# Kernel optimization log

Hardware: AMD Instinct MI355X
Metric: run time of the kernel (lower is better)

The kernel has to match this reference:

```python
import jax, jax.numpy as jnp
import numpy as np

N = 100000   # nodes
E = 300000   # edges
D_IN = 128   # input feature dim
H = 256      # hidden dim
L = 4        # GIN layers
G = 512      # graphs in batch
BN_EPS = 1e-5


def setup_inputs() -> dict:
    key = jax.random.key(0)
    ks = jax.random.split(key, 12)
    s = 0.02
    return {
        "x": jax.random.normal(ks[0], (N, D_IN), jnp.float32),
        "edge_index": jax.random.randint(ks[1], (2, E), 0, N, dtype=jnp.int32),
        "batch": jnp.sort(jax.random.randint(ks[2], (N,), 0, G, dtype=jnp.int32)),
        "W_in": jax.random.normal(ks[3], (D_IN, H), jnp.float32) * s,
        "b_in": jnp.zeros((H,), jnp.float32),
        "eps": jnp.zeros((L,), jnp.float32),           # GINConv train_eps init = 0
        "W1": jax.random.normal(ks[4], (L, H, 2 * H), jnp.float32) * s,
        "b1": jnp.zeros((L, 2 * H), jnp.float32),
        "W2": jax.random.normal(ks[5], (L, 2 * H, H), jnp.float32) * s,
        "b2": jnp.zeros((L, H), jnp.float32),
        "gamma": jnp.ones((L, H), jnp.float32),
        "beta": jnp.zeros((L, H), jnp.float32),
        "Wp1": jax.random.normal(ks[6], (H, H // 2), jnp.float32) * s,
        "bp1": jnp.zeros((H // 2,), jnp.float32),
        "Wp2": jax.random.normal(ks[7], (H // 2, 1), jnp.float32) * s,
        "bp2": jnp.zeros((1,), jnp.float32),
    }


def reference(x, edge_index, batch, W_in, b_in, eps, W1, b1, W2, b2,
              gamma, beta, Wp1, bp1, Wp2, bp2):
    src, dst = edge_index[0], edge_index[1]

    # input projection + relu
    h = jax.nn.relu(x @ W_in + b_in)  # [N, H]

    def layer(h, p):
        e, w1, bb1, w2, bb2, g, bt = p
        # GINConv: sum-aggregate neighbor messages at destination nodes
        agg = jax.ops.segment_sum(h[src], dst, num_segments=N)  # [N, H]
        z = (1.0 + e) * h + agg
        # GIN MLP: H -> 2H -> H
        z = jax.nn.relu(z @ w1 + bb1) @ w2 + bb2
        # BatchNorm over node dim (training-mode batch statistics, biased var)
        mu = jnp.mean(z, axis=0)
        var = jnp.var(z, axis=0)
        z = g * (z - mu) * jax.lax.rsqrt(var + BN_EPS) + bt
        return jax.nn.relu(z), None

    h, _ = jax.lax.scan(layer, h, (eps, W1, b1, W2, b2, gamma, beta))

    # global mean pool per graph
    sums = jax.ops.segment_sum(h, batch, num_segments=G)                       # [G, H]
    counts = jax.ops.segment_sum(jnp.ones((N, 1), h.dtype), batch, num_segments=G)
    pooled = sums / jnp.maximum(counts, 1.0)

    # predictor head (dropout is identity in eval)
    out = jax.nn.relu(pooled @ Wp1 + bp1) @ Wp2 + bp2  # [G, 1]
    return out
```

## Files before the change

kernel.cpp:

```cpp
#include <hip/hip_runtime.h>

#define NN 100000
#define NP 100096
#define EE 300000
#define DIN 128
#define HD  256
#define HD2 512
#define NL  4
#define NG  512
#define BN_EPS 1e-5f

typedef __attribute__((ext_vector_type(8))) short s8v;
typedef __attribute__((ext_vector_type(4))) float f4v;

typedef unsigned short ushort_t;

static __device__ inline ushort_t f2bf(float f) {
    unsigned u = __float_as_uint(f);
    unsigned r = (u + 0x7fffu + ((u >> 16) & 1u)) >> 16;
    return (ushort_t)r;
}
static __device__ inline float bf2f(ushort_t h) {
    return __uint_as_float(((unsigned)h) << 16);
}
static __device__ inline float blo(unsigned v) { return __uint_as_float(v << 16); }
static __device__ inline float bhi(unsigned v) { return __uint_as_float(v & 0xffff0000u); }

#define GLOAD_LDS16(g, l) __builtin_amdgcn_global_load_lds( \
    (const __attribute__((address_space(1))) unsigned int*)(const void*)(g), \
    (__attribute__((address_space(3))) unsigned int*)(void*)(l), 16, 0, 0)

#define WAITCNT_VM8 0xF78
#define WAITCNT_VM4 0xF74
#define WAITCNT_VM0 0xF70

__global__ __launch_bounds__(256) void pack_w1_kernel(
    const float* __restrict__ W1, ushort_t* __restrict__ W1P)
{
    const int t = threadIdx.x, L = t & 63;
    const int gu = blockIdx.x * 4 + (t >> 6);
    const int l = gu >> 8, rem = gu & 255;
    const int c = rem >> 4, u = rem & 15;
    const int kk = u >> 1, nt = u & 1;
    const int h  = c * 32 + nt * 16 + (L & 15);
    const int k0 = kk * 32 + (L >> 4) * 8;
    const float* src = W1 + (size_t)l * HD * HD2;
    s8v v;
#pragma unroll
    for (int e = 0; e < 8; ++e)
        v[e] = (short)f2bf(src[(size_t)(k0 + e) * HD2 + h]);
    *(s8v*)(W1P + (size_t)gu * 512 + L * 8) = v;
}

__global__ __launch_bounds__(256) void pack_w2_kernel(
    const float* __restrict__ W2, ushort_t* __restrict__ W2P)
{
    const int t = threadIdx.x, L = t & 63;
    const int gu = blockIdx.x * 4 + (t >> 6);
    const int l = gu >> 8, rem = gu & 255;
    const int c = rem >> 4, nt = rem & 15;
    const int h  = nt * 16 + (L & 15);
    const int k0 = c * 32 + (L >> 4) * 8;
    const float* src = W2 + (size_t)l * HD2 * HD;
    s8v v;
#pragma unroll
    for (int e = 0; e < 8; ++e)
        v[e] = (short)f2bf(src[(size_t)(k0 + e) * HD + h]);
    *(s8v*)(W2P + (size_t)gu * 512 + L * 8) = v;
}

__global__ __launch_bounds__(256) void pack_win_kernel(
    const float* __restrict__ Win, ushort_t* __restrict__ WinP)
{
    const int t = threadIdx.x, L = t & 63;
    const int gu = blockIdx.x * 4 + (t >> 6);
    const int kk = gu >> 4, nt = gu & 15;
    const int h  = nt * 16 + (L & 15);
    const int k0 = kk * 32 + (L >> 4) * 8;
    s8v v;
#pragma unroll
    for (int e = 0; e < 8; ++e)
        v[e] = (short)f2bf(Win[(size_t)(k0 + e) * HD + h]);
    *(s8v*)(WinP + (size_t)gu * 512 + L * 8) = v;
}

__global__ __launch_bounds__(512, 2) void inproj_kernel(
    const float* __restrict__ x,
    const ushort_t* __restrict__ WinP,
    const float* __restrict__ bias,
    ushort_t* __restrict__ C)
{
    extern __shared__ char smem[];
    ushort_t* Ws = (ushort_t*)smem;
    const int tid = threadIdx.x;
    const int w   = tid >> 6;
    const int L   = tid & 63;
    const int lm  = L & 15;
    const int q   = L >> 4;
    const int row0 = blockIdx.x * 128;

#pragma unroll
    for (int i = 0; i < 8; ++i) {
        const int u = w * 8 + i;
        GLOAD_LDS16(WinP + u * 512 + L * 8, Ws + u * 512);
    }

    const int row = row0 + w * 16 + lm;
    const float* xr = x + (size_t)min(row, NN - 1) * DIN;
    s8v a[4];
#pragma unroll
    for (int kk = 0; kk < 4; ++kk) {
        const float4 u0 = *(const float4*)(xr + kk * 32 + q * 8);
        const float4 u1 = *(const float4*)(xr + kk * 32 + q * 8 + 4);
        s8v v;
        v[0] = (short)f2bf(u0.x); v[1] = (short)f2bf(u0.y);
        v[2] = (short)f2bf(u0.z); v[3] = (short)f2bf(u0.w);
        v[4] = (short)f2bf(u1.x); v[5] = (short)f2bf(u1.y);
        v[6] = (short)f2bf(u1.z); v[7] = (short)f2bf(u1.w);
        a[kk] = v;
    }
    __builtin_amdgcn_s_waitcnt(WAITCNT_VM0);
    __syncthreads();

    f4v acc[16] = {};
#pragma unroll
    for (int kk = 0; kk < 4; ++kk) {
#pragma unroll
        for (int nt = 0; nt < 16; ++nt) {
            s8v b = *(const s8v*)&Ws[(kk * 16 + nt) * 512 + L * 8];
            acc[nt] = __builtin_amdgcn_mfma_f32_16x16x32_bf16(a[kk], b, acc[nt], 0, 0, 0);
        }
    }
    __syncthreads();

    ushort_t* Cs = Ws;
#pragma unroll
    for (int nt = 0; nt < 16; ++nt) {
        const float bj = bias[nt * 16 + lm];
#pragma unroll
        for (int r = 0; r < 4; ++r) {
            const int rr = w * 16 + q * 4 + r;
            Cs[rr * 256 + nt * 16 + lm] = f2bf(fmaxf(acc[nt][r] + bj, 0.f));
        }
    }
    __syncthreads();
#pragma unroll
    for (int i = 0; i < 8; ++i) {
        const int idx = i * 512 + tid;
        const int rr = idx >> 5, ch = idx & 31;
        const s8v v = *(const s8v*)&Cs[idx * 8];
        *(s8v*)(C + (size_t)(row0 + rr) * HD + ch * 8) = v;
    }
}

__global__ __launch_bounds__(512, 4) void fused_mlp_kernel(
    const ushort_t* __restrict__ A,
    const ushort_t* __restrict__ W1l,
    const float*    __restrict__ b1l,
    const ushort_t* __restrict__ W2l,
    const float*    __restrict__ b2l,
    ushort_t* __restrict__ C,
    float* __restrict__ stats)
{
    extern __shared__ char smem[];
    ushort_t* lds = (ushort_t*)smem;
    const int tid = threadIdx.x;
    const int w   = tid >> 6;
    const int L   = tid & 63;
    const int lm  = L & 15;
    const int q   = L >> 4;
    const int row0 = blockIdx.x * 128;

    float* b1s = (float*)(smem + 75776);
    char*  hcb = smem + 65536 + w * 1280;

    if (tid < HD2) b1s[tid] = b1l[tid];
    __syncthreads();

    const ushort_t* Arow = A + (size_t)(row0 + w * 16 + lm) * HD;
    s8v a[8];
#pragma unroll
    for (int kk = 0; kk < 8; ++kk)
        a[kk] = *(const s8v*)(Arow + kk * 32 + q * 8);
    __builtin_amdgcn_s_waitcnt(WAITCNT_VM0);

#define STAGE_W(buf, cc) do {                                                 \
    ushort_t* Wb_ = lds + (buf) * 16384;                                      \
    if (w < 4) {                                                              \
        _Pragma("unroll")                                                     \
        for (int i_ = 0; i_ < 4; ++i_) {                                      \
            const int u_ = w * 4 + i_;                                        \
            GLOAD_LDS16(W1l + ((cc) * 16 + u_) * 512 + L * 8,                 \
                        Wb_ + u_ * 512);                                      \
        }                                                                     \
    } else {                                                                  \
        _Pragma("unroll")                                                     \
        for (int i_ = 0; i_ < 4; ++i_) {                                      \
            const int u_ = (w - 4) * 4 + i_;                                  \
            GLOAD_LDS16(W2l + ((cc) * 16 + u_) * 512 + L * 8,                 \
                        Wb_ + 8192 + u_ * 512);                               \
        }                                                                     \
    }                                                                         \
} while (0)

    STAGE_W(0, 0);
    STAGE_W(1, 1);

    f4v acc2[16] = {};
    for (int c = 0; c < 16; ++c) {
        if (c < 15) __builtin_amdgcn_s_waitcnt(WAITCNT_VM4);
        else        __builtin_amdgcn_s_waitcnt(WAITCNT_VM0);
        __builtin_amdgcn_s_barrier();
        __builtin_amdgcn_sched_barrier(0);

        const ushort_t* Wb  = lds + (c & 1) * 16384;
        const ushort_t* W2b = Wb + 8192;

        f4v acc1[2] = {};
        __builtin_amdgcn_s_setprio(1);
#pragma unroll
        for (int kk = 0; kk < 8; ++kk) {
#pragma unroll
            for (int nt = 0; nt < 2; ++nt) {
                s8v b = *(const s8v*)&Wb[(kk * 2 + nt) * 512 + L * 8];
                acc1[nt] = __builtin_amdgcn_mfma_f32_16x16x32_bf16(a[kk], b, acc1[nt], 0, 0, 0);
            }
        }
        __builtin_amdgcn_s_setprio(0);

#pragma unroll
        for (int nt = 0; nt < 2; ++nt) {
            const float bj = b1s[c * 32 + nt * 16 + lm];
#pragma unroll
            for (int r = 0; r < 4; ++r) {
                const int rr = q * 4 + r;
                *(ushort_t*)(hcb + rr * 80 + (nt * 16 + lm) * 2) =
                    f2bf(fmaxf(acc1[nt][r] + bj, 0.f));
            }
        }
        const s8v at = *(const s8v*)(hcb + lm * 80 + q * 16);
        __builtin_amdgcn_s_setprio(1);
#pragma unroll
        for (int nt = 0; nt < 16; ++nt) {
            s8v b = *(const s8v*)&W2b[nt * 512 + L * 8];
            acc2[nt] = __builtin_amdgcn_mfma_f32_16x16x32_bf16(at, b, acc2[nt], 0, 0, 0);
        }
        __builtin_amdgcn_s_setprio(0);

        __builtin_amdgcn_sched_barrier(0);
        __builtin_amdgcn_s_barrier();
        if (c + 2 < 16) STAGE_W((c & 1), c + 2);
    }
#undef STAGE_W

    __syncthreads();

    ushort_t* Cs = lds;
    float* ssum  = (float*)(smem + 65536);
    float* ssq   = (float*)(smem + 73728);

#pragma unroll
    for (int nt = 0; nt < 16; ++nt) {
        const float bj = b2l[nt * 16 + lm];
        float s = 0.f, sq = 0.f;
#pragma unroll
        for (int r = 0; r < 4; ++r) {
            const float f  = acc2[nt][r] + bj;
            const int row  = w * 16 + q * 4 + r;
            Cs[row * 256 + nt * 16 + lm] = f2bf(f);
            if (row0 + row < NN) { s += f; sq += f * f; }
        }
        s  += __shfl_xor(s, 16, 64);  s  += __shfl_xor(s, 32, 64);
        sq += __shfl_xor(sq, 16, 64); sq += __shfl_xor(sq, 32, 64);
        if (q == 0) {
            ssum[w * 256 + nt * 16 + lm] = s;
            ssq [w * 256 + nt * 16 + lm] = sq;
        }
    }
    __syncthreads();

#pragma unroll
    for (int i = 0; i < 8; ++i) {
        const int idx = i * 512 + tid;
        const int row = idx >> 5, ch = idx & 31;
        const s8v v = *(const s8v*)&Cs[idx * 8];
        *(s8v*)(C + (size_t)(row0 + row) * HD + ch * 8) = v;
    }
    if (tid < HD) {
        float s = 0.f, sq = 0.f;
#pragma unroll
        for (int ww = 0; ww < 8; ++ww) {
            s  += ssum[ww * 256 + tid];
            sq += ssq [ww * 256 + tid];
        }
        unsafeAtomicAdd(&stats[tid], s);
        unsafeAtomicAdd(&stats[HD + tid], sq);
    }
}

__global__ __launch_bounds__(256) void zero_kernel(float* __restrict__ p, long n4)
{
    const long i = (long)blockIdx.x * 256 + threadIdx.x;
    if (i < n4) ((float4*)p)[i] = make_float4(0.f, 0.f, 0.f, 0.f);
}

__global__ __launch_bounds__(256) void init_bn_kernel(
    float* __restrict__ sscale, float* __restrict__ sshift,
    float* __restrict__ stats)
{
    const int t = threadIdx.x;
    sscale[t] = 1.f;
    sshift[t] = 0.f;
    stats[t] = 0.f;
    stats[HD + t] = 0.f;
}

__global__ __launch_bounds__(256) void bnprep_kernel(
    float* __restrict__ stats, const float* __restrict__ gamma,
    const float* __restrict__ beta, float* __restrict__ sscale,
    float* __restrict__ sshift, int Nn)
{
    const int t = threadIdx.x;
    const float invN = 1.0f / (float)Nn;
    const float mu  = stats[t] * invN;
    const float var = stats[HD + t] * invN - mu * mu;
    const float inv = rsqrtf(var + BN_EPS);
    const float sc  = gamma[t] * inv;
    sscale[t] = sc;
    sshift[t] = beta[t] - mu * sc;
    stats[t] = 0.f;
    stats[HD + t] = 0.f;
}

__global__ __launch_bounds__(256) void hist_kernel(
    const int* __restrict__ dst, int* __restrict__ deg, int E)
{
    const int e = blockIdx.x * 256 + threadIdx.x;
    if (e < E) atomicAdd(&deg[dst[e]], 1);
}

__global__ __launch_bounds__(256) void scan1_kernel(
    const int* __restrict__ deg, int* __restrict__ partial,
    int* __restrict__ bsums, int n)
{
    __shared__ int tmp[256];
    const int i = blockIdx.x * 256 + threadIdx.x;
    const int v = (i < n) ? deg[i] : 0;
    tmp[threadIdx.x] = v;
    __syncthreads();
    for (int off = 1; off < 256; off <<= 1) {
        const int t = (threadIdx.x >= off) ? tmp[threadIdx.x - off] : 0;
        __syncthreads();
        tmp[threadIdx.x] += t;
        __syncthreads();
    }
    if (i < n) partial[i] = tmp[threadIdx.x] - v;
    if (threadIdx.x == 255) bsums[blockIdx.x] = tmp[255];
}

__global__ __launch_bounds__(512) void scan2_kernel(int* __restrict__ bsums, int nb)
{
    __shared__ int tmp[512];
    const int i = threadIdx.x;
    const int v = (i < nb) ? bsums[i] : 0;
    tmp[i] = v;
    __syncthreads();
    for (int off = 1; off < 512; off <<= 1) {
        const int t = (i >= off) ? tmp[i - off] : 0;
        __syncthreads();
        tmp[i] += t;
        __syncthreads();
    }
    if (i < nb) bsums[i] = tmp[i] - v;
}

__global__ __launch_bounds__(256) void scan3_kernel(
    const int* __restrict__ partial, const int* __restrict__ bsums,
    int* __restrict__ offs, int* __restrict__ cursor, int n)
{
    const int i = blockIdx.x * 256 + threadIdx.x;
    if (i < n) {
        const int o = partial[i] + bsums[blockIdx.x];
        offs[i] = o;
        cursor[i] = o;
    }
}

__global__ __launch_bounds__(256) void scatter_kernel(
    const int* __restrict__ src, const int* __restrict__ dst,
    int* __restrict__ cursor, int* __restrict__ srcSorted, int E)
{
    const int e = blockIdx.x * 256 + threadIdx.x;
    if (e >= E) return;
    const int p = atomicAdd(&cursor[dst[e]], 1);
    srcSorted[p] = src[e];
}

__global__ __launch_bounds__(256) void aggregate_kernel(
    const ushort_t* __restrict__ z, const int* __restrict__ offs,
    const int* __restrict__ deg, const int* __restrict__ srcSorted,
    const float* __restrict__ epsArr, int epsIdx,
    const float* __restrict__ sscale, const float* __restrict__ sshift,
    ushort_t* __restrict__ out)
{
    const int n = blockIdx.x * 8 + (threadIdx.x >> 5);
    const int L = threadIdx.x & 31;
    const int c0 = L * 8;
    const float4 scA = *(const float4*)(sscale + c0);
    const float4 scB = *(const float4*)(sscale + c0 + 4);
    const float4 shA = *(const float4*)(sshift + c0);
    const float4 shB = *(const float4*)(sshift + c0 + 4);
    const int start = offs[n];
    const int dc = deg[n];
    float a[8] = {};
    float b[8] = {};
    int j = 0;
    for (; j + 1 < dc; j += 2) {
        const int s0 = srcSorted[start + j];
        const int s1 = srcSorted[start + j + 1];
        const uint4 u = *(const uint4*)(z + (size_t)s0 * HD + c0);
        const uint4 v = *(const uint4*)(z + (size_t)s1 * HD + c0);
        a[0] += fmaxf(blo(u.x) * scA.x + shA.x, 0.f);
        a[1] += fmaxf(bhi(u.x) * scA.y + shA.y, 0.f);
        a[2] += fmaxf(blo(u.y) * scA.z + shA.z, 0.f);
        a[3] += fmaxf(bhi(u.y) * scA.w + shA.w, 0.f);
        a[4] += fmaxf(blo(u.z) * scB.x + shB.x, 0.f);
        a[5] += fmaxf(bhi(u.z) * scB.y + shB.y, 0.f);
        a[6] += fmaxf(blo(u.w) * scB.z + shB.z, 0.f);
        a[7] += fmaxf(bhi(u.w) * scB.w + shB.w, 0.f);
        b[0] += fmaxf(blo(v.x) * scA.x + shA.x, 0.f);
        b[1] += fmaxf(bhi(v.x) * scA.y + shA.y, 0.f);
        b[2] += fmaxf(blo(v.y) * scA.z + shA.z, 0.f);
        b[3] += fmaxf(bhi(v.y) * scA.w + shA.w, 0.f);
        b[4] += fmaxf(blo(v.z) * scB.x + shB.x, 0.f);
        b[5] += fmaxf(bhi(v.z) * scB.y + shB.y, 0.f);
        b[6] += fmaxf(blo(v.w) * scB.z + shB.z, 0.f);
        b[7] += fmaxf(bhi(v.w) * scB.w + shB.w, 0.f);
    }
    if (j < dc) {
        const int s0 = srcSorted[start + j];
        const uint4 u = *(const uint4*)(z + (size_t)s0 * HD + c0);
        a[0] += fmaxf(blo(u.x) * scA.x + shA.x, 0.f);
        a[1] += fmaxf(bhi(u.x) * scA.y + shA.y, 0.f);
        a[2] += fmaxf(blo(u.y) * scA.z + shA.z, 0.f);
        a[3] += fmaxf(bhi(u.y) * scA.w + shA.w, 0.f);
        a[4] += fmaxf(blo(u.z) * scB.x + shB.x, 0.f);
        a[5] += fmaxf(bhi(u.z) * scB.y + shB.y, 0.f);
        a[6] += fmaxf(blo(u.w) * scB.z + shB.z, 0.f);
        a[7] += fmaxf(bhi(u.w) * scB.w + shB.w, 0.f);
    }
#pragma unroll
    for (int k = 0; k < 8; ++k) a[k] += b[k];
    const float se = 1.0f + epsArr[epsIdx];
    const uint4 hs = *(const uint4*)(z + (size_t)n * HD + c0);
    float y[8];
    y[0] = se * fmaxf(blo(hs.x) * scA.x + shA.x, 0.f) + a[0];
    y[1] = se * fmaxf(bhi(hs.x) * scA.y + shA.y, 0.f) + a[1];
    y[2] = se * fmaxf(blo(hs.y) * scA.z + shA.z, 0.f) + a[2];
    y[3] = se * fmaxf(bhi(hs.y) * scA.w + shA.w, 0.f) + a[3];
    y[4] = se * fmaxf(blo(hs.z) * scB.x + shB.x, 0.f) + a[4];
    y[5] = se * fmaxf(bhi(hs.z) * scB.y + shB.y, 0.f) + a[5];
    y[6] = se * fmaxf(blo(hs.w) * scB.z + shB.z, 0.f) + a[6];
    y[7] = se * fmaxf(bhi(hs.w) * scB.w + shB.w, 0.f) + a[7];
    uint4 o;
    o.x = (unsigned)f2bf(y[0]) | ((unsigned)f2bf(y[1]) << 16);
    o.y = (unsigned)f2bf(y[2]) | ((unsigned)f2bf(y[3]) << 16);
    o.z = (unsigned)f2bf(y[4]) | ((unsigned)f2bf(y[5]) << 16);
    o.w = (unsigned)f2bf(y[6]) | ((unsigned)f2bf(y[7]) << 16);
    *(uint4*)(out + (size_t)n * HD + c0) = o;
}

__global__ __launch_bounds__(256) void pool_head_kernel(
    const ushort_t* __restrict__ z, const int* __restrict__ batch,
    const float* __restrict__ sscale, const float* __restrict__ sshift,
    const float* __restrict__ Wp1, const float* __restrict__ bp1,
    const float* __restrict__ Wp2, const float* __restrict__ bp2,
    float* __restrict__ out)
{
    __shared__ float poolw[4][HD];
    __shared__ float pool[HD];
    __shared__ float red[128];
    __shared__ int seg[2];
    const int g = blockIdx.x;
    const int t = threadIdx.x;
    const int w = t >> 6;
    const int L = t & 63;
    if (t == 0) {
        int lo = 0, hi = NN;
        while (lo < hi) { const int m = (lo + hi) >> 1; if (batch[m] < g) lo = m + 1; else hi = m; }
        seg[0] = lo;
        hi = NN;
        while (lo < hi) { const int m = (lo + hi) >> 1; if (batch[m] < g + 1) lo = m + 1; else hi = m; }
        seg[1] = lo;
    }
    __syncthreads();
    const int start = seg[0], end = seg[1];
    const int c0 = L * 4;
    const float4 sc = *(const float4*)(sscale + c0);
    const float4 sh = *(const float4*)(sshift + c0);
    float a0 = 0.f, a1 = 0.f, a2 = 0.f, a3 = 0.f;
    float b0 = 0.f, b1 = 0.f, b2 = 0.f, b3 = 0.f;
    int r = start + w;
    for (; r + 4 < end; r += 8) {
        const ushort4 u = *(const ushort4*)(z + (size_t)r * HD + c0);
        const ushort4 v = *(const ushort4*)(z + (size_t)(r + 4) * HD + c0);
        a0 += fmaxf(bf2f(u.x) * sc.x + sh.x, 0.f);
        a1 += fmaxf(bf2f(u.y) * sc.y + sh.y, 0.f);
        a2 += fmaxf(bf2f(u.z) * sc.z + sh.z, 0.f);
        a3 += fmaxf(bf2f(u.w) * sc.w + sh.w, 0.f);
        b0 += fmaxf(bf2f(v.x) * sc.x + sh.x, 0.f);
        b1 += fmaxf(bf2f(v.y) * sc.y + sh.y, 0.f);
        b2 += fmaxf(bf2f(v.z) * sc.z + sh.z, 0.f);
        b3 += fmaxf(bf2f(v.w) * sc.w + sh.w, 0.f);
    }
    if (r < end) {
        const ushort4 u = *(const ushort4*)(z + (size_t)r * HD + c0);
        a0 += fmaxf(bf2f(u.x) * sc.x + sh.x, 0.f);
        a1 += fmaxf(bf2f(u.y) * sc.y + sh.y, 0.f);
        a2 += fmaxf(bf2f(u.z) * sc.z + sh.z, 0.f);
        a3 += fmaxf(bf2f(u.w) * sc.w + sh.w, 0.f);
    }
    poolw[w][c0 + 0] = a0 + b0;
    poolw[w][c0 + 1] = a1 + b1;
    poolw[w][c0 + 2] = a2 + b2;
    poolw[w][c0 + 3] = a3 + b3;
    __syncthreads();
    const float invC = 1.0f / (float)max(end - start, 1);
    pool[t] = (poolw[0][t] + poolw[1][t] + poolw[2][t] + poolw[3][t]) * invC;
    __syncthreads();
    if (t < 128) {
        float acc = 0.f;
#pragma unroll 4
        for (int k = 0; k < HD; ++k)
            acc += pool[k] * Wp1[k * 128 + t];
        red[t] = fmaxf(acc + bp1[t], 0.f) * Wp2[t];
    }
    __syncthreads();
    for (int sft = 64; sft > 0; sft >>= 1) {
        if (t < sft) red[t] += red[t + sft];
        __syncthreads();
    }
    if (t == 0) out[g] = red[0] + bp2[0];
}

extern "C" void kernel_launch(void* const* d_in, const int* in_sizes, int n_in,
                              void* d_out, int out_size, void* d_ws, size_t ws_size,
                              hipStream_t stream)
{
    const float* x     = (const float*)d_in[0];
    const int*   ei    = (const int*)  d_in[1];
    const int*   batch = (const int*)  d_in[2];
    const float* W_in  = (const float*)d_in[3];
    const float* b_in  = (const float*)d_in[4];
    const float* eps   = (const float*)d_in[5];
    const float* W1    = (const float*)d_in[6];
    const float* b1    = (const float*)d_in[7];
    const float* W2    = (const float*)d_in[8];
    const float* b2    = (const float*)d_in[9];
    const float* gamma = (const float*)d_in[10];
    const float* beta  = (const float*)d_in[11];
    const float* Wp1   = (const float*)d_in[12];
    const float* bp1   = (const float*)d_in[13];
    const float* Wp2   = (const float*)d_in[14];
    const float* bp2   = (const float*)d_in[15];

    const int* srcIdx = ei;
    const int* dstIdx = ei + EE;

    char* p = (char*)d_ws;
    ushort_t* zbuf    = (ushort_t*)p;  p += (size_t)NP * HD  * 2;
    ushort_t* abuf    = (ushort_t*)p;  p += (size_t)NP * HD  * 2;
    ushort_t* W1P     = (ushort_t*)p;  p += (size_t)NL * HD2 * HD * 2;
    ushort_t* W2P     = (ushort_t*)p;  p += (size_t)NL * HD * HD2 * 2;
    ushort_t* WinP    = (ushort_t*)p;  p += (size_t)HD * DIN * 2;
    int* deg          = (int*)p;       p += (size_t)NN * 4;
    int* partial      = (int*)p;       p += (size_t)NN * 4;
    int* bsums        = (int*)p;       p += 512 * 4;
    int* offs         = (int*)p;       p += (size_t)NN * 4;
    int* cursor       = (int*)p;       p += (size_t)NN * 4;
    int* srcSorted    = (int*)p;       p += (size_t)EE * 4;
    float* stats      = (float*)p;     p += 2 * HD * 4;
    float* sscale     = (float*)p;     p += HD * 4;
    float* sshift     = (float*)p;     p += HD * 4;

    const int nb = (NN + 255) / 256;
    const int INPROJ_LDS = 65536;
    const int FUSED_LDS  = 81920;

    init_bn_kernel<<<1, 256, 0, stream>>>(sscale, sshift, stats);

    pack_win_kernel<<<16, 256, 0, stream>>>(W_in, WinP);
    pack_w1_kernel<<<256, 256, 0, stream>>>(W1, W1P);
    pack_w2_kernel<<<256, 256, 0, stream>>>(W2, W2P);

    zero_kernel<<<(NN / 4 + 255) / 256, 256, 0, stream>>>((float*)deg, NN / 4);
    hist_kernel<<<(EE + 255) / 256, 256, 0, stream>>>(dstIdx, deg, EE);
    scan1_kernel<<<nb, 256, 0, stream>>>(deg, partial, bsums, NN);
    scan2_kernel<<<1, 512, 0, stream>>>(bsums, nb);
    scan3_kernel<<<nb, 256, 0, stream>>>(partial, bsums, offs, cursor, NN);
    scatter_kernel<<<(EE + 255) / 256, 256, 0, stream>>>(srcIdx, dstIdx, cursor, srcSorted, EE);

    inproj_kernel<<<NP / 128, 512, INPROJ_LDS, stream>>>(x, WinP, b_in, zbuf);

    for (int l = 0; l < NL; ++l) {
        aggregate_kernel<<<NN / 8, 256, 0, stream>>>(
            zbuf, offs, deg, srcSorted, eps, l, sscale, sshift, abuf);

        fused_mlp_kernel<<<NP / 128, 512, FUSED_LDS, stream>>>(
            abuf, W1P + (size_t)l * HD2 * HD, b1 + (size_t)l * HD2,
            W2P + (size_t)l * HD * HD2, b2 + (size_t)l * HD, zbuf, stats);

        bnprep_kernel<<<1, 256, 0, stream>>>(
            stats, gamma + (size_t)l * HD, beta + (size_t)l * HD, sscale, sshift, NN);
    }

    pool_head_kernel<<<NG, 256, 0, stream>>>(zbuf, batch, sscale, sshift,
                                             Wp1, bp1, Wp2, bp2, (float*)d_out);
}
```

Measured before the change: 726.6 us.

## Fold BN prep into aggregate and pool kernels, split neighbor gather across two half-waves

Removes the separate bnprep kernel per layer. Each aggregate block, and the pool head, now computes BN scale and shift from per-layer stats buffers into LDS, which removes four tiny launches and their serialization. Aggregation now uses 64 threads per node, with two half-waves each taking alternate edges and combining through a cross-lane shuffle. This raises memory-level parallelism for the irregular gathers, at the cost of redundant BN math in every block and half the lanes sitting idle on the store.

```diff
diff --git a/kernel.cpp b/kernel.cpp
--- a/kernel.cpp
+++ b/kernel.cpp
@@ -25,6 +25,19 @@
 }
 static __device__ inline float blo(unsigned v) { return __uint_as_float(v << 16); }
 static __device__ inline float bhi(unsigned v) { return __uint_as_float(v & 0xffff0000u); }
+
+static __device__ inline void gacc(float* A, const uint4 u,
+                                   const float4 s0, const float4 s1,
+                                   const float4 h0, const float4 h1, float wg) {
+    A[0] += wg * fmaxf(blo(u.x) * s0.x + h0.x, 0.f);
+    A[1] += wg * fmaxf(bhi(u.x) * s0.y + h0.y, 0.f);
+    A[2] += wg * fmaxf(blo(u.y) * s0.z + h0.z, 0.f);
+    A[3] += wg * fmaxf(bhi(u.y) * s0.w + h0.w, 0.f);
+    A[4] += wg * fmaxf(blo(u.z) * s1.x + h1.x, 0.f);
+    A[5] += wg * fmaxf(bhi(u.z) * s1.y + h1.y, 0.f);
+    A[6] += wg * fmaxf(blo(u.w) * s1.z + h1.z, 0.f);
+    A[7] += wg * fmaxf(bhi(u.w) * s1.w + h1.w, 0.f);
+}
 
 #define GLOAD_LDS16(g, l) __builtin_amdgcn_global_load_lds( \
     (const __attribute__((address_space(1))) unsigned int*)(const void*)(g), \
@@ -304,32 +317,11 @@
     if (i < n4) ((float4*)p)[i] = make_float4(0.f, 0.f, 0.f, 0.f);
 }
 
-__global__ __launch_bounds__(256) void init_bn_kernel(
-    float* __restrict__ sscale, float* __restrict__ sshift,
-    float* __restrict__ stats)
+__global__ __launch_bounds__(256) void init_stats_kernel(float* __restrict__ stats)
 {
     const int t = threadIdx.x;
-    sscale[t] = 1.f;
-    sshift[t] = 0.f;
-    stats[t] = 0.f;
-    stats[HD + t] = 0.f;
-}
-
-__global__ __launch_bounds__(256) void bnprep_kernel(
-    float* __restrict__ stats, const float* __restrict__ gamma,
-    const float* __restrict__ beta, float* __restrict__ sscale,
-    float* __restrict__ sshift, int Nn)
-{
-    const int t = threadIdx.x;
-    const float invN = 1.0f / (float)Nn;
-    const float mu  = stats[t] * invN;
-    const float var = stats[HD + t] * invN - mu * mu;
-    const float inv = rsqrtf(var + BN_EPS);
-    const float sc  = gamma[t] * inv;
-    sscale[t] = sc;
-    sshift[t] = beta[t] - mu * sc;
-    stats[t] = 0.f;
-    stats[HD + t] = 0.f;
+#pragma unroll
+    for (int i = 0; i < 2 * NL; ++i) stats[i * HD + t] = 0.f;
 }
 
 __global__ __launch_bounds__(256) void hist_kernel(
@@ -396,87 +388,89 @@
     srcSorted[p] = src[e];
 }
 
-__global__ __launch_bounds__(256) void aggregate_kernel(
+__global__ __launch_bounds__(512) void aggregate_kernel(
     const ushort_t* __restrict__ z, const int* __restrict__ offs,
     const int* __restrict__ deg, const int* __restrict__ srcSorted,
     const float* __restrict__ epsArr, int epsIdx,
-    const float* __restrict__ sscale, const float* __restrict__ sshift,
+    const float* __restrict__ statsPrev,
+    const float* __restrict__ gammaPrev, const float* __restrict__ betaPrev,
     ushort_t* __restrict__ out)
 {
-    const int n = blockIdx.x * 8 + (threadIdx.x >> 5);
-    const int L = threadIdx.x & 31;
-    const int c0 = L * 8;
-    const float4 scA = *(const float4*)(sscale + c0);
-    const float4 scB = *(const float4*)(sscale + c0 + 4);
-    const float4 shA = *(const float4*)(sshift + c0);
-    const float4 shB = *(const float4*)(sshift + c0 + 4);
+    __shared__ float ssc[HD];
+    __shared__ float ssh[HD];
+    const int t = threadIdx.x;
+    if (t < HD) {
+        float sc = 1.f, sh = 0.f;
+        if (statsPrev) {
+            const float invN = 1.0f / (float)NN;
+            const float mu  = statsPrev[t] * invN;
+            const float var = statsPrev[HD + t] * invN - mu * mu;
+            const float inv = rsqrtf(var + BN_EPS);
+            sc = gammaPrev[t] * inv;
+            sh = betaPrev[t] - mu * sc;
+        }
+        ssc[t] = sc;
+        ssh[t] = sh;
+    }
+    __syncthreads();
+
+    const int n = blockIdx.x * 8 + (t >> 6);
+    const int L = t & 63;
+    const int h = L >> 5;
+    const int c0 = (L & 31) * 8;
+    const float4 scA = *(const float4*)(ssc + c0);
+    const float4 scB = *(const float4*)(ssc + c0 + 4);
+    const float4 shA = *(const float4*)(ssh + c0);
+    const float4 shB = *(const float4*)(ssh + c0 + 4);
     const int start = offs[n];
     const int dc = deg[n];
     float a[8] = {};
     float b[8] = {};
-    int j = 0;
-    for (; j + 1 < dc; j += 2) {
+    int j = h;
+    for (; j + 2 < dc; j += 4) {
         const int s0 = srcSorted[start + j];
-        const int s1 = srcSorted[start + j + 1];
+        const int s1 = srcSorted[start + j + 2];
         const uint4 u = *(const uint4*)(z + (size_t)s0 * HD + c0);
         const uint4 v = *(const uint4*)(z + (size_t)s1 * HD + c0);
-        a[0] += fmaxf(blo(u.x) * scA.x + shA.x, 0.f);
-        a[1] += fmaxf(bhi(u.x) * scA.y + shA.y, 0.f);
-        a[2] += fmaxf(blo(u.y) * scA.z + shA.z, 0.f);
-        a[3] += fmaxf(bhi(u.y) * scA.w + shA.w, 0.f);
-        a[4] += fmaxf(blo(u.z) * scB.x + shB.x, 0.f);
-        a[5] += fmaxf(bhi(u.z) * scB.y + shB.y, 0.f);
-        a[6] += fmaxf(blo(u.w) * scB.z + shB.z, 0.f);
-        a[7] += fmaxf(bhi(u.w) * scB.w + shB.w, 0.f);
-        b[0] += fmaxf(blo(v.x) * scA.x + shA.x, 0.f);
-        b[1] += fmaxf(bhi(v.x) * scA.y + shA.y, 0.f);
-        b[2] += fmaxf(blo(v.y) * scA.z + shA.z, 0.f);
-        b[3] += fmaxf(bhi(v.y) * scA.w + shA.w, 0.f);
-        b[4] += fmaxf(blo(v.z) * scB.x + shB.x, 0.f);
-        b[5] += fmaxf(bhi(v.z) * scB.y + shB.y, 0.f);
-        b[6] += fmaxf(blo(v.w) * scB.z + shB.z, 0.f);
-        b[7] += fmaxf(bhi(v.w) * scB.w + shB.w, 0.f);
+        gacc(a, u, scA, scB, shA, shB, 1.f);
+        gacc(b, v, scA, scB, shA, shB, 1.f);
     }
     if (j < dc) {
         const int s0 = srcSorted[start + j];
         const uint4 u = *(const uint4*)(z + (size_t)s0 * HD + c0);
-        a[0] += fmaxf(blo(u.x) * scA.x + shA.x, 0.f);
-        a[1] += fmaxf(bhi(u.x) * scA.y + shA.y, 0.f);
-        a[2] += fmaxf(blo(u.y) * scA.z + shA.z, 0.f);
-        a[3] += fmaxf(bhi(u.y) * scA.w + shA.w, 0.f);
-        a[4] += fmaxf(blo(u.z) * scB.x + shB.x, 0.f);
-        a[5] += fmaxf(bhi(u.z) * scB.y + shB.y, 0.f);
-        a[6] += fmaxf(blo(u.w) * scB.z + shB.z, 0.f);
-        a[7] += fmaxf(bhi(u.w) * scB.w + shB.w, 0.f);
+        gacc(a, u, scA, scB, shA, shB, 1.f);
     }
 #pragma unroll
     for (int k = 0; k < 8; ++k) a[k] += b[k];
+#pragma unroll
+    for (int k = 0; k < 8; ++k) a[k] += __shfl_xor(a[k], 32, 64);
+
     const float se = 1.0f + epsArr[epsIdx];
     const uint4 hs = *(const uint4*)(z + (size_t)n * HD + c0);
     float y[8];
-    y[0] = se * fmaxf(blo(hs.x) * scA.x + shA.x, 0.f) + a[0];
-    y[1] = se * fmaxf(bhi(hs.x) * scA.y + shA.y, 0.f) + a[1];
-    y[2] = se * fmaxf(blo(hs.y) * scA.z + shA.z, 0.f) + a[2];
-    y[3] = se * fmaxf(bhi(hs.y) * scA.w + shA.w, 0.f) + a[3];
-    y[4] = se * fmaxf(blo(hs.z) * scB.x + shB.x, 0.f) + a[4];
-    y[5] = se * fmaxf(bhi(hs.z) * scB.y + shB.y, 0.f) + a[5];
-    y[6] = se * fmaxf(blo(hs.w) * scB.z + shB.z, 0.f) + a[6];
-    y[7] = se * fmaxf(bhi(hs.w) * scB.w + shB.w, 0.f) + a[7];
-    uint4 o;
-    o.x = (unsigned)f2bf(y[0]) | ((unsigned)f2bf(y[1]) << 16);
-    o.y = (unsigned)f2bf(y[2]) | ((unsigned)f2bf(y[3]) << 16);
-    o.z = (unsigned)f2bf(y[4]) | ((unsigned)f2bf(y[5]) << 16);
-    o.w = (unsigned)f2bf(y[6]) | ((unsigned)f2bf(y[7]) << 16);
-    *(uint4*)(out + (size_t)n * HD + c0) = o;
+#pragma unroll
+    for (int k = 0; k < 8; ++k) y[k] = a[k];
+    gacc(y, hs, scA, scB, shA, shB, se);
+    if (h == 0) {
+        uint4 o;
+        o.x = (unsigned)f2bf(y[0]) | ((unsigned)f2bf(y[1]) << 16);
+        o.y = (unsigned)f2bf(y[2]) | ((unsigned)f2bf(y[3]) << 16);
+        o.z = (unsigned)f2bf(y[4]) | ((unsigned)f2bf(y[5]) << 16);
+        o.w = (unsigned)f2bf(y[6]) | ((unsigned)f2bf(y[7]) << 16);
+        *(uint4*)(out + (size_t)n * HD + c0) = o;
+    }
 }
 
 __global__ __launch_bounds__(256) void pool_head_kernel(
     const ushort_t* __restrict__ z, const int* __restrict__ batch,
-    const float* __restrict__ sscale, const float* __restrict__ sshift,
+    const float* __restrict__ statsPrev,
+    const float* __restrict__ gammaPrev, const float* __restrict__ betaPrev,
     const float* __restrict__ Wp1, const float* __restrict__ bp1,
     const float* __restrict__ Wp2, const float* __restrict__ bp2,
     float* __restrict__ out)
 {
+    __shared__ float ssc[HD];
+    __shared__ float ssh[HD];
     __shared__ float poolw[4][HD];
     __shared__ float pool[HD];
     __shared__ float red[128];
@@ -485,6 +479,15 @@
     const int t = threadIdx.x;
     const int w = t >> 6;
     const int L = t & 63;
+    {
+        const float invN = 1.0f / (float)NN;
+        const float mu  = statsPrev[t] * invN;
+        const float var = statsPrev[HD + t] * invN - mu * mu;
+        const float inv = rsqrtf(var + BN_EPS);
+        const float sc  = gammaPrev[t] * inv;
+        ssc[t] = sc;
+        ssh[t] = betaPrev[t] - mu * sc;
+    }
     if (t == 0) {
         int lo = 0, hi = NN;
         while (lo < hi) { const int m = (lo + hi) >> 1; if (batch[m] < g) lo = m + 1; else hi = m; }
@@ -496,8 +499,8 @@
     __syncthreads();
     const int start = seg[0], end = seg[1];
     const int c0 = L * 4;
-    const float4 sc = *(const float4*)(sscale + c0);
-    const float4 sh = *(const float4*)(sshift + c0);
+    const float4 sc = *(const float4*)(ssc + c0);
+    const float4 sh = *(const float4*)(ssh + c0);
     float a0 = 0.f, a1 = 0.f, a2 = 0.f, a3 = 0.f;
     float b0 = 0.f, b1 = 0.f, b2 = 0.f, b3 = 0.f;
     int r = start + w;
@@ -579,15 +582,13 @@
     int* offs         = (int*)p;       p += (size_t)NN * 4;
     int* cursor       = (int*)p;       p += (size_t)NN * 4;
     int* srcSorted    = (int*)p;       p += (size_t)EE * 4;
-    float* stats      = (float*)p;     p += 2 * HD * 4;
-    float* sscale     = (float*)p;     p += HD * 4;
-    float* sshift     = (float*)p;     p += HD * 4;
+    float* stats      = (float*)p;     p += (size_t)NL * 2 * HD * 4;
 
     const int nb = (NN + 255) / 256;
     const int INPROJ_LDS = 65536;
     const int FUSED_LDS  = 81920;
 
-    init_bn_kernel<<<1, 256, 0, stream>>>(sscale, sshift, stats);
+    init_stats_kernel<<<1, 256, 0, stream>>>(stats);
 
     pack_win_kernel<<<16, 256, 0, stream>>>(W_in, WinP);
     pack_w1_kernel<<<256, 256, 0, stream>>>(W1, W1P);
@@ -603,17 +604,20 @@
     inproj_kernel<<<NP / 128, 512, INPROJ_LDS, stream>>>(x, WinP, b_in, zbuf);
 
     for (int l = 0; l < NL; ++l) {
-        aggregate_kernel<<<NN / 8, 256, 0, stream>>>(
-            zbuf, offs, deg, srcSorted, eps, l, sscale, sshift, abuf);
+        const float* sp = (l == 0) ? nullptr : stats + (size_t)(l - 1) * 2 * HD;
+        aggregate_kernel<<<NN / 8, 512, 0, stream>>>(
+            zbuf, offs, deg, srcSorted, eps, l,
+            sp, gamma + (size_t)(l - 1 < 0 ? 0 : l - 1) * HD,
+            beta + (size_t)(l - 1 < 0 ? 0 : l - 1) * HD, abuf);
 
         fused_mlp_kernel<<<NP / 128, 512, FUSED_LDS, stream>>>(
             abuf, W1P + (size_t)l * HD2 * HD, b1 + (size_t)l * HD2,
-            W2P + (size_t)l * HD * HD2, b2 + (size_t)l * HD, zbuf, stats);
-
-        bnprep_kernel<<<1, 256, 0, stream>>>(
-            stats, gamma + (size_t)l * HD, beta + (size_t)l * HD, sscale, sshift, NN);
-    }
-
-    pool_head_kernel<<<NG, 256, 0, stream>>>(zbuf, batch, sscale, sshift,
-                                             Wp1, bp1, Wp2, bp2, (float*)d_out);
-}
+            W2P + (size_t)l * HD * HD2, b2 + (size_t)l * HD, zbuf,
+            stats + (size_t)l * 2 * HD);
+    }
+
+    pool_head_kernel<<<NG, 256, 0, stream>>>(
+        zbuf, batch, stats + (size_t)(NL - 1) * 2 * HD,
+        gamma + (size_t)(NL - 1) * HD, beta + (size_t)(NL - 1) * HD,
+        Wp1, bp1, Wp2, bp2, (float*)d_out);
+}
```

New measurement: 783.3 us. 7.8% more time.
